# Kernel optimization log

Measured on AMD Instinct MI355X. Metric: run time of the kernel, lower is better.

Reference implementation:

```python
import jax, jax.numpy as jnp
import numpy as np

B, L, D = 2048, 64, 300   # batch, words per sentence, embedding dim (== kernel_size)
C = 512                    # conv out_channels
H, O = 2048, 1             # fc hidden, fc output


def setup_inputs() -> dict:
    key = jax.random.key(0)
    ks = jax.random.split(key, 8)
    s = 0.05
    return {
        "x1": jax.random.normal(ks[0], (B, L, D), jnp.float32),
        "x2": jax.random.normal(ks[1], (B, L, D), jnp.float32),
        # Conv1d(in=1, out=C, kernel=D) weight is [C,1,D]; stored as [C,D]
        "Wc": jax.random.normal(ks[2], (C, D), jnp.float32) * s,
        "bc": jax.random.normal(ks[3], (C,), jnp.float32) * s,
        "W1": jax.random.normal(ks[4], (H, 2 * C), jnp.float32) * s,
        "b1": jax.random.normal(ks[5], (H,), jnp.float32) * s,
        "W2": jax.random.normal(ks[6], (O, H), jnp.float32) * s,
        "b2": jax.random.normal(ks[7], (O,), jnp.float32) * s,
    }


def reference(x1, x2, Wc, bc, W1, b1, W2, b2):
    # Per-word Conv1d(kernel=D) + ReLU is a full-width filter == linear map D->C.
    # Batch all words in one einsum instead of the original Python loop.
    def encode(x):
        h = jax.nn.relu(jnp.einsum('bld,cd->blc', x, Wc) + bc)  # [B,L,C]
        return jnp.max(h, axis=1)                                # max over words -> [B,C]

    e1 = encode(x1)
    e2 = encode(x2)
    feat = jnp.concatenate([e1 - e2, e1 * e2], axis=1)           # [B,2C]
    h = jnp.tanh(feat @ W1.T + b1)                               # [B,H]
    return h @ W2.T + b2                                         # [B,O]
```

## Files before the change

### kernel.cpp

```cpp
#include <hip/hip_runtime.h>


#define B_SZ 2048
#define L_SZ 64
#define D_SZ 300
#define C_SZ 512
#define H_SZ 2048
#define NKC 40

typedef __bf16 bf16x8 __attribute__((ext_vector_type(8)));
typedef float f32x4 __attribute__((ext_vector_type(4)));

__device__ __forceinline__ unsigned short f2bf(float f) {
  unsigned int u = __float_as_uint(f);
  u += 0x7fffu + ((u >> 16) & 1u);
  return (unsigned short)(u >> 16);
}

__device__ __forceinline__ bf16x8 cvt8(float4 v0, float4 v1) {
  bf16x8 r;
  r[0] = (__bf16)v0.x; r[1] = (__bf16)v0.y; r[2] = (__bf16)v0.z; r[3] = (__bf16)v0.w;
  r[4] = (__bf16)v1.x; r[5] = (__bf16)v1.y; r[6] = (__bf16)v1.z; r[7] = (__bf16)v1.w;
  return r;
}

__global__ __launch_bounds__(256)
void convert_kernel(const float* __restrict__ Wc, const float* __restrict__ W1,
                    unsigned short* __restrict__ WcSwz, unsigned short* __restrict__ W1Swz) {
  int id = blockIdx.x * 256 + threadIdx.x;
  if (id < C_SZ * NKC) {
    int c = id / NKC, kc = id - c * NKC;
    unsigned short tmp[8];
    #pragma unroll
    for (int i = 0; i < 8; ++i) {
      int k = kc * 8 + i;
      tmp[i] = (k < D_SZ) ? f2bf(Wc[c * D_SZ + k]) : (unsigned short)0;
    }
    unsigned short* dst = WcSwz + (((c >> 4) * NKC + kc) * 16 + (c & 15)) * 8;
    *reinterpret_cast<uint4*>(dst) = *reinterpret_cast<uint4*>(tmp);
    return;
  }
  id -= C_SZ * NKC;
  if (id < H_SZ * 128) {
    int j = id >> 7, kc = id & 127;
    const float* src = W1 + (size_t)j * 1024 + kc * 8;
    unsigned short tmp[8];
    #pragma unroll
    for (int i = 0; i < 8; ++i) tmp[i] = f2bf(src[i]);
    unsigned short* dst = W1Swz + (((j >> 4) * 128 + kc) * 16 + (j & 15)) * 8;
    *reinterpret_cast<uint4*>(dst) = *reinterpret_cast<uint4*>(tmp);
  }
}

__global__ __launch_bounds__(256, 2)
void encode_kernel(const float* __restrict__ x1, const float* __restrict__ x2,
                   const unsigned short* __restrict__ WcSwz,
                   const float* __restrict__ bc, float* __restrict__ e) {
  const int b = blockIdx.x, z = blockIdx.y;
  const float* __restrict__ x = (z ? x2 : x1) + (size_t)b * (L_SZ * D_SZ);
  const int tid = threadIdx.x;
  const int wave = tid >> 6, lane = tid & 63;
  const int l16 = lane & 15, quad = lane >> 4;

  const float* rowp[4];
  #pragma unroll
  for (int mt = 0; mt < 4; ++mt)
    rowp[mt] = x + (mt * 16 + l16) * D_SZ + quad * 8;

  f32x4 acc[4][8];
  #pragma unroll
  for (int mt = 0; mt < 4; ++mt)
    #pragma unroll
    for (int nt = 0; nt < 8; ++nt)
      #pragma unroll
      for (int r = 0; r < 4; ++r) acc[mt][nt][r] = 0.f;

  #pragma unroll
  for (int ks = 0; ks < 10; ++ks) {
    bf16x8 a[4];
    #pragma unroll
    for (int mt = 0; mt < 4; ++mt) {
      float4 v0, v1;
      if (ks < 9) {
        v0 = *reinterpret_cast<const float4*>(rowp[mt] + ks * 32);
        v1 = *reinterpret_cast<const float4*>(rowp[mt] + ks * 32 + 4);
      } else {
        v0 = make_float4(0.f, 0.f, 0.f, 0.f);
        v1 = v0;
        if (quad < 2)  v0 = *reinterpret_cast<const float4*>(rowp[mt] + 288);
        if (quad == 0) v1 = *reinterpret_cast<const float4*>(rowp[mt] + 292);
      }
      a[mt] = cvt8(v0, v1);
    }
    #pragma unroll
    for (int nt = 0; nt < 8; ++nt) {
      const unsigned short* bp =
          WcSwz + ((((wave * 8 + nt) * NKC) + ks * 4 + quad) * 16 + l16) * 8;
      bf16x8 bw = *reinterpret_cast<const bf16x8*>(bp);
      #pragma unroll
      for (int mt = 0; mt < 4; ++mt)
        acc[mt][nt] = __builtin_amdgcn_mfma_f32_16x16x32_bf16(a[mt], bw, acc[mt][nt], 0, 0, 0);
    }
  }

  #pragma unroll
  for (int nt = 0; nt < 8; ++nt) {
    int c = wave * 128 + nt * 16 + l16;
    float bias = bc[c];
    float v = 0.f;
    #pragma unroll
    for (int mt = 0; mt < 4; ++mt)
      #pragma unroll
      for (int r = 0; r < 4; ++r)
        v = fmaxf(v, acc[mt][nt][r] + bias);
    v = fmaxf(v, __shfl_xor(v, 16));
    v = fmaxf(v, __shfl_xor(v, 32));
    if (quad == 0)
      e[((size_t)z * B_SZ + b) * C_SZ + c] = v;
  }
}

__global__ __launch_bounds__(256)
void feat_kernel(const float* __restrict__ e, unsigned short* __restrict__ featSwz) {
  int id = blockIdx.x * 256 + threadIdx.x;
  if (id >= B_SZ * 128) return;
  int b = id >> 7, kc = id & 127;
  unsigned short tmp[8];
  #pragma unroll
  for (int i = 0; i < 8; ++i) {
    int k = kc * 8 + i, c = k & 511;
    float a = e[(size_t)b * C_SZ + c];
    float bb = e[(size_t)B_SZ * C_SZ + (size_t)b * C_SZ + c];
    tmp[i] = f2bf((k < C_SZ) ? (a - bb) : (a * bb));
  }
  unsigned short* dst = featSwz + (((b >> 4) * 128 + kc) * 16 + (b & 15)) * 8;
  *reinterpret_cast<uint4*>(dst) = *reinterpret_cast<uint4*>(tmp);
}

__global__ __launch_bounds__(256, 4)
void fc1_kernel(const unsigned short* __restrict__ featSwz,
                const unsigned short* __restrict__ W1Swz,
                const float* __restrict__ b1, const float* __restrict__ W2,
                float* __restrict__ partial) {
  const int mbase = blockIdx.x * 32;
  const int tid = threadIdx.x;
  const int wave = tid >> 6, lane = tid & 63;
  const int l16 = lane & 15, quad = lane >> 4;
  const int nbase = blockIdx.y * 128 + wave * 32;

  f32x4 acc[2][2];
  #pragma unroll
  for (int mt = 0; mt < 2; ++mt)
    #pragma unroll
    for (int nt = 0; nt < 2; ++nt)
      #pragma unroll
      for (int r = 0; r < 4; ++r) acc[mt][nt][r] = 0.f;

  #pragma unroll 4
  for (int ks = 0; ks < 32; ++ks) {
    bf16x8 a[2], bw[2];
    #pragma unroll
    for (int mt = 0; mt < 2; ++mt)
      a[mt] = *reinterpret_cast<const bf16x8*>(
          featSwz + (((size_t)(blockIdx.x * 2 + mt) * 128 + ks * 4 + quad) * 16 + l16) * 8);
    #pragma unroll
    for (int nt = 0; nt < 2; ++nt)
      bw[nt] = *reinterpret_cast<const bf16x8*>(
          W1Swz + (((size_t)(blockIdx.y * 8 + wave * 2 + nt) * 128 + ks * 4 + quad) * 16 + l16) * 8);
    #pragma unroll
    for (int mt = 0; mt < 2; ++mt)
      #pragma unroll
      for (int nt = 0; nt < 2; ++nt)
        acc[mt][nt] = __builtin_amdgcn_mfma_f32_16x16x32_bf16(a[mt], bw[nt], acc[mt][nt], 0, 0, 0);
  }

  float c[2][4];
  #pragma unroll
  for (int mt = 0; mt < 2; ++mt)
    #pragma unroll
    for (int r = 0; r < 4; ++r) c[mt][r] = 0.f;

  #pragma unroll
  for (int nt = 0; nt < 2; ++nt) {
    int j = nbase + nt * 16 + l16;
    float bias = b1[j];
    float w2 = W2[j];
    #pragma unroll
    for (int mt = 0; mt < 2; ++mt)
      #pragma unroll
      for (int r = 0; r < 4; ++r) {
        float pre = acc[mt][nt][r] + bias;
        pre = fminf(fmaxf(pre, -15.f), 15.f);
        float ex = __expf(2.f * pre);
        c[mt][r] += w2 * ((ex - 1.f) / (ex + 1.f));
      }
  }
  #pragma unroll
  for (int off = 1; off <= 8; off <<= 1)
    #pragma unroll
    for (int mt = 0; mt < 2; ++mt)
      #pragma unroll
      for (int r = 0; r < 4; ++r)
        c[mt][r] += __shfl_xor(c[mt][r], off);

  if (l16 == 0) {
    int slice = blockIdx.y * 4 + wave;
    #pragma unroll
    for (int mt = 0; mt < 2; ++mt)
      #pragma unroll
      for (int r = 0; r < 4; ++r) {
        int brow = mbase + mt * 16 + quad * 4 + r;
        partial[(size_t)slice * B_SZ + brow] = c[mt][r];
      }
  }
}

__global__ __launch_bounds__(256)
void finalize_kernel(const float* __restrict__ partial, const float* __restrict__ b2,
                     float* __restrict__ out) {
  int b = blockIdx.x * 256 + threadIdx.x;
  float s = b2[0];
  #pragma unroll 8
  for (int i = 0; i < 64; ++i) s += partial[(size_t)i * B_SZ + b];
  out[b] = s;
}

extern "C" void kernel_launch(void* const* d_in, const int* in_sizes, int n_in,
                              void* d_out, int out_size, void* d_ws, size_t ws_size,
                              hipStream_t stream) {
  const float* x1 = (const float*)d_in[0];
  const float* x2 = (const float*)d_in[1];
  const float* Wc = (const float*)d_in[2];
  const float* bc = (const float*)d_in[3];
  const float* W1 = (const float*)d_in[4];
  const float* b1 = (const float*)d_in[5];
  const float* W2 = (const float*)d_in[6];
  const float* b2 = (const float*)d_in[7];

  char* ws = (char*)d_ws;
  unsigned short* WcSwz   = (unsigned short*)(ws);
  unsigned short* W1Swz   = (unsigned short*)(ws + 327680);
  float*          e       = (float*)(ws + 4521984);
  unsigned short* featSwz = (unsigned short*)(ws + 12910592);
  float*          partial = (float*)(ws + 17104896);

  {
    int total = C_SZ * NKC + H_SZ * 128;
    convert_kernel<<<(total + 255) / 256, 256, 0, stream>>>(Wc, W1, WcSwz, W1Swz);
  }
  encode_kernel<<<dim3(B_SZ, 2), 256, 0, stream>>>(x1, x2, WcSwz, bc, e);
  feat_kernel<<<(B_SZ * 128 + 255) / 256, 256, 0, stream>>>(e, featSwz);
  fc1_kernel<<<dim3(B_SZ / 32, H_SZ / 128), 256, 0, stream>>>(featSwz, W1Swz, b1, W2, partial);
  finalize_kernel<<<B_SZ / 256, 256, 0, stream>>>(partial, b2, (float*)d_out);
}
```

Before: 515.8 us.

## Fuse encode and feature kernels with LDS double-buffered persistent tiles; atomic fc2 reduce

Replaces the per-sentence encode kernel and the separate feat kernel with a persistent 256-block encoder. Each block loops over 16 sentence tiles (x1/x2 pairs), prefetches the next tile into registers, stages it as bf16 in double-buffered LDS, and writes the swizzled bf16 feature rows directly. It also removes the finalize kernel: the output is seeded with b2 in the convert kernel and fc1 accumulates through atomicAdd. The aim is to cut launches and intermediate global traffic and to overlap loads with MFMA. The cost is fewer blocks (256) and more barriers, which may limit parallelism, plus nondeterministic atomic summation order.

New measurement: 563.0 us. 9.2% more time.

```diff
diff --git a/kernel.cpp b/kernel.cpp
--- a/kernel.cpp
+++ b/kernel.cpp
@@ -17,17 +17,13 @@
   return (unsigned short)(u >> 16);
 }
 
-__device__ __forceinline__ bf16x8 cvt8(float4 v0, float4 v1) {
-  bf16x8 r;
-  r[0] = (__bf16)v0.x; r[1] = (__bf16)v0.y; r[2] = (__bf16)v0.z; r[3] = (__bf16)v0.w;
-  r[4] = (__bf16)v1.x; r[5] = (__bf16)v1.y; r[6] = (__bf16)v1.z; r[7] = (__bf16)v1.w;
-  return r;
-}
-
 __global__ __launch_bounds__(256)
 void convert_kernel(const float* __restrict__ Wc, const float* __restrict__ W1,
-                    unsigned short* __restrict__ WcSwz, unsigned short* __restrict__ W1Swz) {
+                    const float* __restrict__ b2,
+                    unsigned short* __restrict__ WcSwz, unsigned short* __restrict__ W1Swz,
+                    float* __restrict__ out) {
   int id = blockIdx.x * 256 + threadIdx.x;
+  if (id < B_SZ) out[id] = b2[0];
   if (id < C_SZ * NKC) {
     int c = id / NKC, kc = id - c * NKC;
     unsigned short tmp[8];
@@ -52,96 +48,140 @@
   }
 }
 
-__global__ __launch_bounds__(256, 2)
-void encode_kernel(const float* __restrict__ x1, const float* __restrict__ x2,
-                   const unsigned short* __restrict__ WcSwz,
-                   const float* __restrict__ bc, float* __restrict__ e) {
-  const int b = blockIdx.x, z = blockIdx.y;
-  const float* __restrict__ x = (z ? x2 : x1) + (size_t)b * (L_SZ * D_SZ);
+__global__ __launch_bounds__(512, 2)
+void encode_feat_kernel(const float* __restrict__ x1, const float* __restrict__ x2,
+                        const unsigned short* __restrict__ WcSwz,
+                        const float* __restrict__ bc,
+                        unsigned short* __restrict__ featSwz) {
+  __shared__ unsigned short xs[2][64 * NKC * 8];
+  __shared__ float fs[1024];
   const int tid = threadIdx.x;
   const int wave = tid >> 6, lane = tid & 63;
   const int l16 = lane & 15, quad = lane >> 4;
 
-  const float* rowp[4];
-  #pragma unroll
-  for (int mt = 0; mt < 4; ++mt)
-    rowp[mt] = x + (mt * 16 + l16) * D_SZ + quad * 8;
-
-  f32x4 acc[4][8];
-  #pragma unroll
-  for (int mt = 0; mt < 4; ++mt)
-    #pragma unroll
-    for (int nt = 0; nt < 8; ++nt)
-      #pragma unroll
-      for (int r = 0; r < 4; ++r) acc[mt][nt][r] = 0.f;
-
-  #pragma unroll
-  for (int ks = 0; ks < 10; ++ks) {
-    bf16x8 a[4];
-    #pragma unroll
-    for (int mt = 0; mt < 4; ++mt) {
-      float4 v0, v1;
-      if (ks < 9) {
-        v0 = *reinterpret_cast<const float4*>(rowp[mt] + ks * 32);
-        v1 = *reinterpret_cast<const float4*>(rowp[mt] + ks * 32 + 4);
-      } else {
-        v0 = make_float4(0.f, 0.f, 0.f, 0.f);
-        v1 = v0;
-        if (quad < 2)  v0 = *reinterpret_cast<const float4*>(rowp[mt] + 288);
-        if (quad == 0) v1 = *reinterpret_cast<const float4*>(rowp[mt] + 292);
-      }
-      a[mt] = cvt8(v0, v1);
-    }
-    #pragma unroll
-    for (int nt = 0; nt < 8; ++nt) {
-      const unsigned short* bp =
-          WcSwz + ((((wave * 8 + nt) * NKC) + ks * 4 + quad) * 16 + l16) * 8;
-      bf16x8 bw = *reinterpret_cast<const bf16x8*>(bp);
+  for (int i = tid; i < 256; i += 512) {
+    int buf = i >> 7, r = i & 127;
+    int mt = r >> 5, kc = 38 + ((r >> 4) & 1), l = r & 15;
+    *reinterpret_cast<uint4*>(&xs[buf][mt * 5120 + kc * 128 + l * 8]) = make_uint4(0, 0, 0, 0);
+  }
+
+  float bias[4];
+  #pragma unroll
+  for (int nt = 0; nt < 4; ++nt) bias[nt] = bc[wave * 64 + nt * 16 + l16];
+
+  float4 pf0[5], pf1[5];
+  auto LOAD = [&](int t) {
+    const float* xb = ((t & 1) ? x2 : x1) +
+                      (size_t)(blockIdx.x + (t >> 1) * 256) * (L_SZ * D_SZ);
+    #pragma unroll
+    for (int r = 0; r < 5; ++r) {
+      int idx = r * 512 + tid;
+      if (idx < 2432) {
+        int g = idx >> 4, l = idx & 15;
+        int mt = g / 38, c8 = g - mt * 38;
+        const float* s = xb + (mt * 16 + l) * D_SZ + c8 * 8;
+        pf0[r] = *reinterpret_cast<const float4*>(s);
+        pf1[r] = (c8 < 37) ? *reinterpret_cast<const float4*>(s + 4)
+                           : make_float4(0.f, 0.f, 0.f, 0.f);
+      }
+    }
+  };
+  auto WRITE = [&](int buf) {
+    #pragma unroll
+    for (int r = 0; r < 5; ++r) {
+      int idx = r * 512 + tid;
+      if (idx < 2432) {
+        int g = idx >> 4, l = idx & 15;
+        int mt = g / 38, c8 = g - mt * 38;
+        unsigned int w0 = (unsigned int)f2bf(pf0[r].x) | ((unsigned int)f2bf(pf0[r].y) << 16);
+        unsigned int w1 = (unsigned int)f2bf(pf0[r].z) | ((unsigned int)f2bf(pf0[r].w) << 16);
+        unsigned int w2 = (unsigned int)f2bf(pf1[r].x) | ((unsigned int)f2bf(pf1[r].y) << 16);
+        unsigned int w3 = (unsigned int)f2bf(pf1[r].z) | ((unsigned int)f2bf(pf1[r].w) << 16);
+        *reinterpret_cast<uint4*>(&xs[buf][mt * 5120 + c8 * 128 + l * 8]) =
+            make_uint4(w0, w1, w2, w3);
+      }
+    }
+  };
+
+  LOAD(0);
+  WRITE(0);
+  __syncthreads();
+
+  const unsigned short* wc_lane = WcSwz + (wave * 4) * 5120 + quad * 128 + l16 * 8;
+  float e1[4];
+  int cur = 0;
+
+  #pragma unroll 2
+  for (int t = 0; t < 16; ++t) {
+    if (t < 15) LOAD(t + 1);
+
+    f32x4 acc[4][4];
+    #pragma unroll
+    for (int mt = 0; mt < 4; ++mt)
+      #pragma unroll
+      for (int nt = 0; nt < 4; ++nt)
+        #pragma unroll
+        for (int r = 0; r < 4; ++r) acc[mt][nt][r] = 0.f;
+
+    const unsigned short* xb = &xs[cur][quad * 128 + l16 * 8];
+    #pragma unroll
+    for (int ks = 0; ks < 10; ++ks) {
+      bf16x8 a[4];
       #pragma unroll
       for (int mt = 0; mt < 4; ++mt)
-        acc[mt][nt] = __builtin_amdgcn_mfma_f32_16x16x32_bf16(a[mt], bw, acc[mt][nt], 0, 0, 0);
-    }
-  }
-
-  #pragma unroll
-  for (int nt = 0; nt < 8; ++nt) {
-    int c = wave * 128 + nt * 16 + l16;
-    float bias = bc[c];
-    float v = 0.f;
-    #pragma unroll
-    for (int mt = 0; mt < 4; ++mt)
-      #pragma unroll
-      for (int r = 0; r < 4; ++r)
-        v = fmaxf(v, acc[mt][nt][r] + bias);
-    v = fmaxf(v, __shfl_xor(v, 16));
-    v = fmaxf(v, __shfl_xor(v, 32));
-    if (quad == 0)
-      e[((size_t)z * B_SZ + b) * C_SZ + c] = v;
-  }
-}
-
-__global__ __launch_bounds__(256)
-void feat_kernel(const float* __restrict__ e, unsigned short* __restrict__ featSwz) {
-  int id = blockIdx.x * 256 + threadIdx.x;
-  if (id >= B_SZ * 128) return;
-  int b = id >> 7, kc = id & 127;
-  unsigned short tmp[8];
-  #pragma unroll
-  for (int i = 0; i < 8; ++i) {
-    int k = kc * 8 + i, c = k & 511;
-    float a = e[(size_t)b * C_SZ + c];
-    float bb = e[(size_t)B_SZ * C_SZ + (size_t)b * C_SZ + c];
-    tmp[i] = f2bf((k < C_SZ) ? (a - bb) : (a * bb));
-  }
-  unsigned short* dst = featSwz + (((b >> 4) * 128 + kc) * 16 + (b & 15)) * 8;
-  *reinterpret_cast<uint4*>(dst) = *reinterpret_cast<uint4*>(tmp);
+        a[mt] = *reinterpret_cast<const bf16x8*>(xb + mt * 5120 + ks * 512);
+      #pragma unroll
+      for (int nt = 0; nt < 4; ++nt) {
+        bf16x8 bw = *reinterpret_cast<const bf16x8*>(wc_lane + nt * 5120 + ks * 512);
+        #pragma unroll
+        for (int mt = 0; mt < 4; ++mt)
+          acc[mt][nt] = __builtin_amdgcn_mfma_f32_16x16x32_bf16(a[mt], bw, acc[mt][nt], 0, 0, 0);
+      }
+    }
+
+    #pragma unroll
+    for (int nt = 0; nt < 4; ++nt) {
+      float v = 0.f;
+      #pragma unroll
+      for (int mt = 0; mt < 4; ++mt)
+        #pragma unroll
+        for (int r = 0; r < 4; ++r)
+          v = fmaxf(v, acc[mt][nt][r] + bias[nt]);
+      v = fmaxf(v, __shfl_xor(v, 16));
+      v = fmaxf(v, __shfl_xor(v, 32));
+      if (!(t & 1)) {
+        e1[nt] = v;
+      } else if (quad == 0) {
+        int c = wave * 64 + nt * 16 + l16;
+        fs[c]       = e1[nt] - v;
+        fs[512 + c] = e1[nt] * v;
+      }
+    }
+
+    __syncthreads();
+
+    if (t & 1) {
+      int b = blockIdx.x + (t >> 1) * 256;
+      if (tid < 128) {
+        unsigned short tmp[8];
+        #pragma unroll
+        for (int i = 0; i < 8; ++i) tmp[i] = f2bf(fs[tid * 8 + i]);
+        *reinterpret_cast<uint4*>(featSwz + (((b >> 4) * 128 + tid) * 16 + (b & 15)) * 8) =
+            *reinterpret_cast<uint4*>(tmp);
+      }
+    }
+    if (t < 15) WRITE(cur ^ 1);
+
+    __syncthreads();
+    cur ^= 1;
+  }
 }
 
 __global__ __launch_bounds__(256, 4)
 void fc1_kernel(const unsigned short* __restrict__ featSwz,
                 const unsigned short* __restrict__ W1Swz,
                 const float* __restrict__ b1, const float* __restrict__ W2,
-                float* __restrict__ partial) {
+                float* __restrict__ out) {
   const int mbase = blockIdx.x * 32;
   const int tid = threadIdx.x;
   const int wave = tid >> 6, lane = tid & 63;
@@ -204,25 +244,14 @@
         c[mt][r] += __shfl_xor(c[mt][r], off);
 
   if (l16 == 0) {
-    int slice = blockIdx.y * 4 + wave;
     #pragma unroll
     for (int mt = 0; mt < 2; ++mt)
       #pragma unroll
       for (int r = 0; r < 4; ++r) {
         int brow = mbase + mt * 16 + quad * 4 + r;
-        partial[(size_t)slice * B_SZ + brow] = c[mt][r];
-      }
-  }
-}
-
-__global__ __launch_bounds__(256)
-void finalize_kernel(const float* __restrict__ partial, const float* __restrict__ b2,
-                     float* __restrict__ out) {
-  int b = blockIdx.x * 256 + threadIdx.x;
-  float s = b2[0];
-  #pragma unroll 8
-  for (int i = 0; i < 64; ++i) s += partial[(size_t)i * B_SZ + b];
-  out[b] = s;
+        atomicAdd(&out[brow], c[mt][r]);
+      }
+  }
 }
 
 extern "C" void kernel_launch(void* const* d_in, const int* in_sizes, int n_in,
@@ -240,16 +269,14 @@
   char* ws = (char*)d_ws;
   unsigned short* WcSwz   = (unsigned short*)(ws);
   unsigned short* W1Swz   = (unsigned short*)(ws + 327680);
-  float*          e       = (float*)(ws + 4521984);
-  unsigned short* featSwz = (unsigned short*)(ws + 12910592);
-  float*          partial = (float*)(ws + 17104896);
+  unsigned short* featSwz = (unsigned short*)(ws + 4521984);
 
   {
     int total = C_SZ * NKC + H_SZ * 128;
-    convert_kernel<<<(total + 255) / 256, 256, 0, stream>>>(Wc, W1, WcSwz, W1Swz);
-  }
-  encode_kernel<<<dim3(B_SZ, 2), 256, 0, stream>>>(x1, x2, WcSwz, bc, e);
-  feat_kernel<<<(B_SZ * 128 + 255) / 256, 256, 0, stream>>>(e, featSwz);
-  fc1_kernel<<<dim3(B_SZ / 32, H_SZ / 128), 256, 0, stream>>>(featSwz, W1Swz, b1, W2, partial);
-  finalize_kernel<<<B_SZ / 256, 256, 0, stream>>>(partial, b2, (float*)d_out);
-}
+    convert_kernel<<<(total + 255) / 256, 256, 0, stream>>>(Wc, W1, b2, WcSwz, W1Swz,
+                                                            (float*)d_out);
+  }
+  encode_feat_kernel<<<256, 512, 0, stream>>>(x1, x2, WcSwz, bc, featSwz);
+  fc1_kernel<<<dim3(B_SZ / 32, H_SZ / 128), 256, 0, stream>>>(featSwz, W1Swz, b1, W2,
+                                                              (float*)d_out);
+}
```
